# Performance work log

Hardware: AMD Instinct MI355X
Metric: run time of the kernel (lower is better)

Reference implementation:

```python
import jax, jax.numpy as jnp
import numpy as np

EMBED_DIM = 1024
NUM_HEADS = 16
HEAD_DIM = EMBED_DIM // NUM_HEADS
MAX_SEQ_LEN = 2048
B, T = 2, 2048


def setup_inputs() -> dict:
    key = jax.random.key(0)
    ks = jax.random.split(key, 12)
    d = EMBED_DIM
    s = lambda fan_in: 1.0 / np.sqrt(fan_in)
    return {
        "x": jax.random.normal(ks[0], (B, T, d), dtype=jnp.float32),
        "ln1_g": jnp.ones((d,), jnp.float32),
        "ln1_b": jnp.zeros((d,), jnp.float32),
        "w_attn": jax.random.normal(ks[1], (d, 3 * d), jnp.float32) * s(d),
        "b_attn": jnp.zeros((3 * d,), jnp.float32),
        "w_proj": jax.random.normal(ks[2], (d, d), jnp.float32) * s(d),
        "b_proj": jnp.zeros((d,), jnp.float32),
        "ln2_g": jnp.ones((d,), jnp.float32),
        "ln2_b": jnp.zeros((d,), jnp.float32),
        "w_fc": jax.random.normal(ks[3], (d, 4 * d), jnp.float32) * s(d),
        "b_fc": jnp.zeros((4 * d,), jnp.float32),
        "w_fc2": jax.random.normal(ks[4], (4 * d, d), jnp.float32) * s(4 * d),
        "b_fc2": jnp.zeros((d,), jnp.float32),
    }


def _layernorm(x, g, b, eps=1e-5):
    mu = jnp.mean(x, axis=-1, keepdims=True)
    var = jnp.var(x, axis=-1, keepdims=True)
    return (x - mu) * jax.lax.rsqrt(var + eps) * g + b


def _attention(x, w_attn, b_attn, w_proj, b_proj):
    b, t, c = x.shape
    qkv = x @ w_attn + b_attn  # [B,T,3C]
    q, k, v = jnp.split(qkv, 3, axis=-1)
    # [B,T,C] -> [B,H,T,Dh]
    rs = lambda a: a.reshape(b, t, NUM_HEADS, HEAD_DIM).transpose(0, 2, 1, 3)
    q, k, v = rs(q), rs(k), rs(v)
    wei = jnp.einsum("bhqd,bhkd->bhqk", q, k) * (HEAD_DIM ** -0.5)
    causal = jnp.tril(jnp.ones((t, t), bool))
    wei = jnp.where(causal, wei, -jnp.inf)
    wei = jax.nn.softmax(wei, axis=-1)  # attn_dropout is identity in eval mode
    out = jnp.einsum("bhqk,bhkd->bhqd", wei, v)
    out = out.transpose(0, 2, 1, 3).reshape(b, t, c)
    return out @ w_proj + b_proj  # resid_dropout identity in eval mode


def _ffn(x, w_fc, b_fc, w_fc2, b_fc2):
    h = jax.nn.gelu(x @ w_fc + b_fc, approximate=False)
    return h @ w_fc2 + b_fc2  # dropout identity in eval mode


def reference(x, ln1_g, ln1_b, w_attn, b_attn, w_proj, b_proj,
              ln2_g, ln2_b, w_fc, b_fc, w_fc2, b_fc2):
    x = x + _attention(_layernorm(x, ln1_g, ln1_b), w_attn, b_attn, w_proj, b_proj)
    x = x + _ffn(_layernorm(x, ln2_g, ln2_b), w_fc, b_fc, w_fc2, b_fc2)
    return x
```

## Files before the change

kernel.cpp:

```cpp
#include <hip/hip_runtime.h>

#define EMBED 1024
#define THREE_EMBED 3072
#define HEADS 16
#define HDIM 64
#define SEQ 2048
#define BATCH 2
#define MTOT 4096

typedef short bf16x8 __attribute__((ext_vector_type(8)));
typedef float f32x4 __attribute__((ext_vector_type(4)));

#define MFMA16(a, b, c) __builtin_amdgcn_mfma_f32_16x16x32_bf16(a, b, c, 0, 0, 0)

__device__ __forceinline__ unsigned short f2bf(float f) {
  union { float f; unsigned int u; } v; v.f = f;
  unsigned int r = v.u + 0x7fffu + ((v.u >> 16) & 1u);
  return (unsigned short)(r >> 16);
}

__device__ __forceinline__ void gload_lds16(const unsigned short* g, unsigned short* l) {
  __builtin_amdgcn_global_load_lds(
      (const __attribute__((address_space(1))) void*)g,
      (__attribute__((address_space(3))) void*)l, 16, 0, 0);
}

__device__ __forceinline__ void wait_vm0_barrier() {
  asm volatile("s_waitcnt vmcnt(0)" ::: "memory");
  __builtin_amdgcn_s_barrier();
}

__global__ __launch_bounds__(256) void k_transpose_bf16(
    const float* __restrict__ in, unsigned short* __restrict__ out, int K, int N) {
  __shared__ float t[32][33];
  int tx = threadIdx.x & 31, ty = threadIdx.x >> 5;
  int n0 = blockIdx.x * 32, k0 = blockIdx.y * 32;
#pragma unroll
  for (int i = 0; i < 32; i += 8)
    t[ty + i][tx] = in[(size_t)(k0 + ty + i) * N + n0 + tx];
  __syncthreads();
#pragma unroll
  for (int i = 0; i < 32; i += 8)
    out[(size_t)(n0 + ty + i) * K + k0 + tx] = f2bf(t[tx][ty + i]);
}

__global__ __launch_bounds__(256) void k_transpose_v(
    const unsigned short* __restrict__ qkv, unsigned short* __restrict__ Vt) {
  __shared__ unsigned short t[32][33];
  int tx = threadIdx.x & 31, ty = threadIdx.x >> 5;
  int t0 = blockIdx.x * 32;
  int d0 = (blockIdx.y & 1) * 32;
  int bh = blockIdx.y >> 1;
  int b = bh >> 4, h = bh & 15;
  const unsigned short* src = qkv + (size_t)b * SEQ * THREE_EMBED + 2 * EMBED + h * HDIM;
#pragma unroll
  for (int i = 0; i < 32; i += 8)
    t[ty + i][tx] = src[(size_t)(t0 + ty + i) * THREE_EMBED + d0 + tx];
  __syncthreads();
  unsigned short* dst = Vt + (size_t)bh * HDIM * SEQ;
#pragma unroll
  for (int i = 0; i < 32; i += 8)
    dst[(size_t)(d0 + ty + i) * SEQ + t0 + tx] = t[tx][ty + i];
}

__global__ __launch_bounds__(256) void k_layernorm(
    const float* __restrict__ x, const float* __restrict__ g,
    const float* __restrict__ b, unsigned short* __restrict__ out) {
  int row = blockIdx.x;
  int tid = threadIdx.x;
  const float4 xv = *(const float4*)(x + (size_t)row * EMBED + tid * 4);
  float s = xv.x + xv.y + xv.z + xv.w;
  float sq = xv.x * xv.x + xv.y * xv.y + xv.z * xv.z + xv.w * xv.w;
#pragma unroll
  for (int off = 1; off < 64; off <<= 1) {
    s += __shfl_xor(s, off);
    sq += __shfl_xor(sq, off);
  }
  __shared__ float red[8];
  int w = tid >> 6;
  if ((tid & 63) == 0) { red[w] = s; red[4 + w] = sq; }
  __syncthreads();
  s = red[0] + red[1] + red[2] + red[3];
  sq = red[4] + red[5] + red[6] + red[7];
  float mu = s * (1.0f / EMBED);
  float var = sq * (1.0f / EMBED) - mu * mu;
  float rs = rsqrtf(var + 1e-5f);
  float xs[4] = {xv.x, xv.y, xv.z, xv.w};
  unsigned short o[4];
#pragma unroll
  for (int c = 0; c < 4; c++) {
    int col = tid * 4 + c;
    o[c] = f2bf((xs[c] - mu) * rs * g[col] + b[col]);
  }
  *(ushort4*)(out + (size_t)row * EMBED + tid * 4) = *(const ushort4*)o;
}

template <int EPI, int BN>
__global__ __launch_bounds__(256) void k_gemm(
    const unsigned short* __restrict__ A, const unsigned short* __restrict__ Bt,
    const float* __restrict__ bias, const float* __restrict__ resid,
    float* __restrict__ outf, unsigned short* __restrict__ outb,
    int M, int N, int K) {
  constexpr int BCH = BN / 16;
  constexpr int CHUNKS = 8 + BCH;
  constexpr int CPW = CHUNKS / 4;
  constexpr int MI = (BN == 128) ? 4 : 2;
  constexpr int NJ = 4;
  __shared__ unsigned short lA[2][128 * 32];
  __shared__ unsigned short lB[2][BN * 32];
  int tid = threadIdx.x;
  int nwg = gridDim.x * gridDim.y;
  int bid = blockIdx.y * gridDim.x + blockIdx.x;
  int swz = (bid & 7) * (nwg >> 3) + (bid >> 3);
  int m0 = (swz / gridDim.x) * 128, n0 = (swz % gridDim.x) * BN;
  int lane = tid & 63, w = tid >> 6;
  int wm = (BN == 128) ? (w >> 1) * 64 : w * 32;
  int wn = (BN == 128) ? (w & 1) * 64 : 0;
  int lr = lane & 15, lg = lane >> 4;
  f32x4 acc[MI][NJ] = {};
  int scol = ((lane & 3) ^ ((lane >> 3) & 3)) * 8;
  const unsigned short* gsrc[CPW];
  int loff[CPW];
  bool isa[CPW];
#pragma unroll
  for (int c0 = 0; c0 < CPW; c0++) {
    int c = w * CPW + c0;
    if (c < 8) {
      int row = c * 16 + (lane >> 2);
      gsrc[c0] = A + (size_t)(m0 + row) * K + scol;
      loff[c0] = c * 512;
      isa[c0] = true;
    } else {
      int row = (c - 8) * 16 + (lane >> 2);
      gsrc[c0] = Bt + (size_t)(n0 + row) * K + scol;
      loff[c0] = (c - 8) * 512;
      isa[c0] = false;
    }
  }
  auto stage = [&](int k0, int cur) {
#pragma unroll
    for (int c0 = 0; c0 < CPW; c0++)
      gload_lds16(gsrc[c0] + k0, isa[c0] ? &lA[cur][loff[c0]] : &lB[cur][loff[c0]]);
  };
  int fcol = (lg ^ ((lr >> 1) & 3)) * 8;
  int nt = K >> 5;
  stage(0, 0);
  wait_vm0_barrier();
  int cur = 0;
  for (int t = 0; t < nt; t++) {
    if (t + 1 < nt) stage((t + 1) * 32, cur ^ 1);
    bf16x8 af[MI], bfr[NJ];
#pragma unroll
    for (int i = 0; i < MI; i++)
      af[i] = *(const bf16x8*)&lA[cur][(wm + i * 16 + lr) * 32 + fcol];
#pragma unroll
    for (int j = 0; j < NJ; j++)
      bfr[j] = *(const bf16x8*)&lB[cur][(wn + j * 16 + lr) * 32 + fcol];
#pragma unroll
    for (int i = 0; i < MI; i++)
#pragma unroll
      for (int j = 0; j < NJ; j++)
        acc[i][j] = MFMA16(af[i], bfr[j], acc[i][j]);
    wait_vm0_barrier();
    cur ^= 1;
  }
#pragma unroll
  for (int i = 0; i < MI; i++) {
#pragma unroll
    for (int j = 0; j < NJ; j++) {
      int colb = n0 + wn + j * 16 + lr;
      float bv = bias[colb];
#pragma unroll
      for (int r = 0; r < 4; r++) {
        int row = m0 + wm + i * 16 + lg * 4 + r;
        float v = acc[i][j][r] + bv;
        size_t idx = (size_t)row * N + colb;
        if constexpr (EPI == 0) {
          outb[idx] = f2bf(v);
        } else if constexpr (EPI == 1) {
          outf[idx] = v + resid[idx];
        } else {
          float gv = 0.5f * v * (1.0f + erff(v * 0.70710678118654752f));
          outb[idx] = f2bf(gv);
        }
      }
    }
  }
}

__global__ __launch_bounds__(256) void k_attention(
    const unsigned short* __restrict__ qkv, const unsigned short* __restrict__ Vt,
    unsigned short* __restrict__ out) {
  __shared__ unsigned short lK[2][64 * 64];
  __shared__ unsigned short lV[2][64 * 64];
  __shared__ unsigned short lP[4][16][72];
  int bid = blockIdx.x;
  int i = bid >> 3;
  int qt = 31 - (i >> 2);
  int bh = (bid & 7) * 4 + (i & 3);
  int b = bh >> 4, h = bh & 15;
  int tid = threadIdx.x, lane = tid & 63, w = tid >> 6;
  int lr = lane & 15, lg = lane >> 4;
  const unsigned short* base = qkv + (size_t)b * SEQ * THREE_EMBED + h * HDIM;
  const unsigned short* Kb = base + EMBED;
  const unsigned short* Vb = Vt + (size_t)bh * HDIM * SEQ;
  int q0 = qt * 64 + w * 16;
  bf16x8 qf[2];
  {
    int qrow = q0 + lr;
    qf[0] = *(const bf16x8*)(base + (size_t)qrow * THREE_EMBED + lg * 8);
    qf[1] = *(const bf16x8*)(base + (size_t)qrow * THREE_EMBED + 32 + lg * 8);
  }
  bf16x8 ones;
  {
    short o1 = 0x3F80;
#pragma unroll
    for (int j = 0; j < 8; j++) ones[j] = o1;
  }
  f32x4 o[4] = {};
  f32x4 osum = {};
  float m_[4] = {-INFINITY, -INFINITY, -INFINITY, -INFINITY};
  int srow = lane >> 3;
  int scol = ((lane & 7) ^ (lane >> 3)) * 8;
  const float SCL = 0.125f * 1.4426950408889634f;
  int nkv = qt + 1;
  auto stage = [&](int kt, int cur) {
#pragma unroll
    for (int c = 0; c < 2; c++) {
      int chunk = w * 2 + c;
      int row = chunk * 8 + srow;
      gload_lds16(Kb + (size_t)(kt * 64 + row) * THREE_EMBED + scol, &lK[cur][chunk * 512]);
      gload_lds16(Vb + (size_t)row * SEQ + kt * 64 + scol, &lV[cur][chunk * 512]);
    }
  };
  stage(0, 0);
  wait_vm0_barrier();
  int cur = 0;
  for (int kt = 0; kt < nkv; kt++) {
    if (kt + 1 < nkv) stage(kt + 1, cur ^ 1);
    __builtin_amdgcn_s_setprio(1);
    f32x4 s[4];
#pragma unroll
    for (int ct = 0; ct < 4; ct++) {
      int krow = ct * 16 + lr;
      int sw = (krow & 7) << 3;
      bf16x8 k0 = *(const bf16x8*)&lK[cur][krow * 64 + ((lg * 8) ^ sw)];
      bf16x8 k1 = *(const bf16x8*)&lK[cur][krow * 64 + ((32 + lg * 8) ^ sw)];
      f32x4 z = {};
      z = MFMA16(qf[0], k0, z);
      s[ct] = MFMA16(qf[1], k1, z);
    }
    __builtin_amdgcn_s_setprio(0);
    bool maskt = (kt * 64 + 63 > q0);
    float pm[4] = {-INFINITY, -INFINITY, -INFINITY, -INFINITY};
#pragma unroll
    for (int ct = 0; ct < 4; ct++) {
#pragma unroll
      for (int r = 0; r < 4; r++) {
        float sv = s[ct][r] * SCL;
        if (maskt) {
          int kg = kt * 64 + ct * 16 + lr;
          int qg = q0 + lg * 4 + r;
          if (kg > qg) sv = -INFINITY;
        }
        s[ct][r] = sv;
        pm[r] = fmaxf(pm[r], sv);
      }
    }
    float dm = fmaxf(fmaxf(pm[0] - m_[0], pm[1] - m_[1]),
                     fmaxf(pm[2] - m_[2], pm[3] - m_[3]));
    if (!__all(dm <= 8.0f)) {
#pragma unroll
      for (int r = 0; r < 4; r++) {
        float mx = pm[r];
        mx = fmaxf(mx, __shfl_xor(mx, 1));
        mx = fmaxf(mx, __shfl_xor(mx, 2));
        mx = fmaxf(mx, __shfl_xor(mx, 4));
        mx = fmaxf(mx, __shfl_xor(mx, 8));
        float mn = fmaxf(m_[r], mx);
        float al = exp2f(m_[r] - mn);
        m_[r] = mn;
        osum[r] *= al;
#pragma unroll
        for (int dt = 0; dt < 4; dt++) o[dt][r] *= al;
      }
    }
#pragma unroll
    for (int ct = 0; ct < 4; ct++)
#pragma unroll
      for (int r = 0; r < 4; r++)
        lP[w][lg * 4 + r][ct * 16 + lr] = f2bf(exp2f(s[ct][r] - m_[r]));
    __builtin_amdgcn_s_setprio(1);
#pragma unroll
    for (int ks = 0; ks < 2; ks++) {
      bf16x8 pf = *(const bf16x8*)&lP[w][lr][ks * 32 + lg * 8];
      osum = MFMA16(pf, ones, osum);
#pragma unroll
      for (int dt = 0; dt < 4; dt++) {
        int vrow = dt * 16 + lr;
        int sw = (vrow & 7) << 3;
        bf16x8 vf = *(const bf16x8*)&lV[cur][vrow * 64 + ((ks * 32 + lg * 8) ^ sw)];
        o[dt] = MFMA16(pf, vf, o[dt]);
      }
    }
    __builtin_amdgcn_s_setprio(0);
    wait_vm0_barrier();
    cur ^= 1;
  }
#pragma unroll
  for (int dt = 0; dt < 4; dt++)
#pragma unroll
    for (int r = 0; r < 4; r++) {
      int row = q0 + lg * 4 + r;
      float val = o[dt][r] / osum[r];
      out[(size_t)(b * SEQ + row) * EMBED + h * HDIM + dt * 16 + lr] = f2bf(val);
    }
}

extern "C" void kernel_launch(void* const* d_in, const int* in_sizes, int n_in,
                              void* d_out, int out_size, void* d_ws, size_t ws_size,
                              hipStream_t stream) {
  const float* x      = (const float*)d_in[0];
  const float* ln1_g  = (const float*)d_in[1];
  const float* ln1_b  = (const float*)d_in[2];
  const float* w_attn = (const float*)d_in[3];
  const float* b_attn = (const float*)d_in[4];
  const float* w_proj = (const float*)d_in[5];
  const float* b_proj = (const float*)d_in[6];
  const float* ln2_g  = (const float*)d_in[7];
  const float* ln2_b  = (const float*)d_in[8];
  const float* w_fc   = (const float*)d_in[9];
  const float* b_fc   = (const float*)d_in[10];
  const float* w_fc2  = (const float*)d_in[11];
  const float* b_fc2  = (const float*)d_in[12];
  float* outp = (float*)d_out;

  char* ws = (char*)d_ws;
  unsigned short* wT_attn = (unsigned short*)(ws);
  unsigned short* wT_proj = (unsigned short*)(ws + 6291456);
  unsigned short* wT_fc   = (unsigned short*)(ws + 8388608);
  unsigned short* wT_fc2  = (unsigned short*)(ws + 16777216);
  unsigned short* buf1    = (unsigned short*)(ws + 25165824);
  float*          x1      = (float*)(ws + 33554432);
  unsigned short* Vt      = (unsigned short*)(ws + 33554432);
  unsigned short* qkv_h   = (unsigned short*)(ws + 50331648);

  dim3 blk(256);
  k_transpose_bf16<<<dim3(3072 / 32, 1024 / 32), blk, 0, stream>>>(w_attn, wT_attn, 1024, 3072);
  k_transpose_bf16<<<dim3(1024 / 32, 1024 / 32), blk, 0, stream>>>(w_proj, wT_proj, 1024, 1024);
  k_transpose_bf16<<<dim3(4096 / 32, 1024 / 32), blk, 0, stream>>>(w_fc, wT_fc, 1024, 4096);
  k_transpose_bf16<<<dim3(1024 / 32, 4096 / 32), blk, 0, stream>>>(w_fc2, wT_fc2, 4096, 1024);
  k_layernorm<<<dim3(MTOT), blk, 0, stream>>>(x, ln1_g, ln1_b, buf1);
  k_gemm<0, 128><<<dim3(THREE_EMBED / 128, MTOT / 128), blk, 0, stream>>>(
      buf1, wT_attn, b_attn, nullptr, nullptr, qkv_h, MTOT, THREE_EMBED, EMBED);
  k_transpose_v<<<dim3(SEQ / 32, 2 * BATCH * HEADS), blk, 0, stream>>>(qkv_h, Vt);
  k_attention<<<dim3(1024), blk, 0, stream>>>(qkv_h, Vt, buf1);
  k_gemm<1, 64><<<dim3(EMBED / 64, MTOT / 128), blk, 0, stream>>>(
      buf1, wT_proj, b_proj, x, x1, nullptr, MTOT, EMBED, EMBED);
  k_layernorm<<<dim3(MTOT), blk, 0, stream>>>(x1, ln2_g, ln2_b, buf1);
  k_gemm<2, 128><<<dim3(4 * EMBED / 128, MTOT / 128), blk, 0, stream>>>(
      buf1, wT_fc, b_fc, nullptr, nullptr, qkv_h, MTOT, 4 * EMBED, EMBED);
  k_gemm<1, 64><<<dim3(EMBED / 64, MTOT / 128), blk, 0, stream>>>(
      qkv_h, wT_fc2, b_fc2, x1, outp, nullptr, MTOT, EMBED, 4 * EMBED);
}
```

Before: 279.3 us.

## Add 256x256-tile 8-wave GEMM with staged prefetch for QKV and FC1

Adds a new GEMM kernel using 256x256 output tiles, 512 threads (8 waves), a K-step of 64 and a swizzled LDS layout. Global-to-LDS loads for the next K tile are split into four stages interleaved with quarter-tile MFMA phases, separated by barriers and s_setprio. It replaces the 128-tile kernel for the QKV projection and the FC1+GELU GEMM, aiming for more operand reuse and better overlap of loads with MFMA. In exchange the grid is smaller (192 and 256 workgroups), which may underfill the GPU's CUs, and the many barriers may stall waves.

```diff
diff --git a/kernel.cpp b/kernel.cpp
--- a/kernel.cpp
+++ b/kernel.cpp
@@ -93,6 +93,140 @@
     o[c] = f2bf((xs[c] - mu) * rs * g[col] + b[col]);
   }
   *(ushort4*)(out + (size_t)row * EMBED + tid * 4) = *(const ushort4*)o;
+}
+
+template <int EPI>
+__global__ __launch_bounds__(512, 2) void k_gemm8(
+    const unsigned short* __restrict__ A, const unsigned short* __restrict__ Bt,
+    const float* __restrict__ bias, const float* __restrict__ resid,
+    float* __restrict__ outf, unsigned short* __restrict__ outb,
+    int M, int N, int K) {
+  __shared__ unsigned short lA[2][16384];
+  __shared__ unsigned short lB[2][16384];
+  int tid = threadIdx.x;
+  int nwg = gridDim.x * gridDim.y;
+  int bid = blockIdx.y * gridDim.x + blockIdx.x;
+  int swz = (bid & 7) * (nwg >> 3) + (bid >> 3);
+  int m0 = (swz / gridDim.x) * 256, n0 = (swz % gridDim.x) * 256;
+  int lane = tid & 63, w = tid >> 6;
+  int lr = lane & 15, lg = lane >> 4;
+  int warow = (w >> 2) * 64;
+  int wbrow = (w & 3) * 32;
+  int rx = lr & 7;
+  int colk[2] = {(lg ^ rx) * 8, ((4 + lg) ^ rx) * 8};
+  f32x4 acc[8][4] = {};
+  int swzk = ((lane & 7) ^ ((lane >> 3) & 7)) * 8;
+  const unsigned short* gA[2];
+  const unsigned short* gB[2];
+#pragma unroll
+  for (int i = 0; i < 2; i++) {
+    int chrow = (w * 2 + i) * 8 + (lane >> 3);
+    gA[i] = A + (size_t)(m0 + chrow) * K + swzk;
+    gB[i] = Bt + (size_t)(n0 + chrow) * K + swzk;
+  }
+  int NT = K >> 6;
+  auto stage1 = [&](int sel, int kt, int nxt) {
+    int h = sel >> 1;
+    size_t goff = (size_t)(h * 128) * K + (size_t)kt * 64;
+    int lo = h * 8192 + w * 1024;
+    if ((sel & 1) == 0) {
+      gload_lds16(gA[0] + goff, &lA[nxt][lo]);
+      gload_lds16(gA[1] + goff, &lA[nxt][lo + 512]);
+    } else {
+      gload_lds16(gB[0] + goff, &lB[nxt][lo]);
+      gload_lds16(gB[1] + goff, &lB[nxt][lo + 512]);
+    }
+  };
+  bf16x8 afr[4][2], bfr[2][2];
+  auto dsrd = [&](int cur, int mh, int nh) {
+#pragma unroll
+    for (int ii = 0; ii < 4; ii++) {
+      int ra = mh * 128 + warow + ii * 16 + lr;
+#pragma unroll
+      for (int ks = 0; ks < 2; ks++)
+        afr[ii][ks] = *(const bf16x8*)&lA[cur][ra * 64 + colk[ks]];
+    }
+#pragma unroll
+    for (int jj = 0; jj < 2; jj++) {
+      int rb = nh * 128 + wbrow + jj * 16 + lr;
+#pragma unroll
+      for (int ks = 0; ks < 2; ks++)
+        bfr[jj][ks] = *(const bf16x8*)&lB[cur][rb * 64 + colk[ks]];
+    }
+  };
+  auto domfma = [&](int mh, int nh) {
+    __builtin_amdgcn_s_setprio(1);
+#pragma unroll
+    for (int ii = 0; ii < 4; ii++)
+#pragma unroll
+      for (int jj = 0; jj < 2; jj++)
+#pragma unroll
+        for (int ks = 0; ks < 2; ks++)
+          acc[mh * 4 + ii][nh * 2 + jj] =
+              MFMA16(afr[ii][ks], bfr[jj][ks], acc[mh * 4 + ii][nh * 2 + jj]);
+    __builtin_amdgcn_s_setprio(0);
+  };
+  stage1(0, 0, 0); stage1(1, 0, 0); stage1(2, 0, 0); stage1(3, 0, 0);
+  wait_vm0_barrier();
+  for (int t = 0; t < NT - 1; t++) {
+    int cur = t & 1, nxt = cur ^ 1;
+    dsrd(cur, 0, 0); stage1(0, t + 1, nxt);
+    asm volatile("s_waitcnt vmcnt(4)" ::: "memory");
+    __builtin_amdgcn_s_barrier();
+    domfma(0, 0);
+    __builtin_amdgcn_s_barrier();
+    dsrd(cur, 1, 0); stage1(1, t + 1, nxt);
+    asm volatile("s_waitcnt vmcnt(4)" ::: "memory");
+    __builtin_amdgcn_s_barrier();
+    domfma(1, 0);
+    __builtin_amdgcn_s_barrier();
+    dsrd(cur, 0, 1); stage1(2, t + 1, nxt);
+    __builtin_amdgcn_s_barrier();
+    domfma(0, 1);
+    __builtin_amdgcn_s_barrier();
+    dsrd(cur, 1, 1); stage1(3, t + 1, nxt);
+    asm volatile("s_waitcnt vmcnt(4)" ::: "memory");
+    __builtin_amdgcn_s_barrier();
+    domfma(1, 1);
+    __builtin_amdgcn_s_barrier();
+  }
+  {
+    int cur = (NT - 1) & 1;
+    dsrd(cur, 0, 0);
+    asm volatile("s_waitcnt vmcnt(2)" ::: "memory");
+    __builtin_amdgcn_s_barrier();
+    domfma(0, 0);
+    __builtin_amdgcn_s_barrier();
+    dsrd(cur, 1, 0);
+    asm volatile("s_waitcnt vmcnt(0)" ::: "memory");
+    __builtin_amdgcn_s_barrier();
+    domfma(1, 0);
+    __builtin_amdgcn_s_barrier();
+    dsrd(cur, 0, 1); domfma(0, 1);
+    dsrd(cur, 1, 1); domfma(1, 1);
+  }
+#pragma unroll
+  for (int i = 0; i < 8; i++) {
+#pragma unroll
+    for (int j = 0; j < 4; j++) {
+      int col = n0 + (j >> 1) * 128 + wbrow + (j & 1) * 16 + lr;
+      float bv = bias[col];
+#pragma unroll
+      for (int r = 0; r < 4; r++) {
+        int row = m0 + (i >> 2) * 128 + warow + (i & 3) * 16 + lg * 4 + r;
+        float v = acc[i][j][r] + bv;
+        size_t idx = (size_t)row * N + col;
+        if constexpr (EPI == 0) {
+          outb[idx] = f2bf(v);
+        } else if constexpr (EPI == 1) {
+          outf[idx] = v + resid[idx];
+        } else {
+          float gv = 0.5f * v * (1.0f + erff(v * 0.70710678118654752f));
+          outb[idx] = f2bf(gv);
+        }
+      }
+    }
+  }
 }
 
 template <int EPI, int BN>
@@ -351,14 +485,14 @@
   k_transpose_bf16<<<dim3(4096 / 32, 1024 / 32), blk, 0, stream>>>(w_fc, wT_fc, 1024, 4096);
   k_transpose_bf16<<<dim3(1024 / 32, 4096 / 32), blk, 0, stream>>>(w_fc2, wT_fc2, 4096, 1024);
   k_layernorm<<<dim3(MTOT), blk, 0, stream>>>(x, ln1_g, ln1_b, buf1);
-  k_gemm<0, 128><<<dim3(THREE_EMBED / 128, MTOT / 128), blk, 0, stream>>>(
+  k_gemm8<0><<<dim3(THREE_EMBED / 256, MTOT / 256), dim3(512), 0, stream>>>(
       buf1, wT_attn, b_attn, nullptr, nullptr, qkv_h, MTOT, THREE_EMBED, EMBED);
   k_transpose_v<<<dim3(SEQ / 32, 2 * BATCH * HEADS), blk, 0, stream>>>(qkv_h, Vt);
   k_attention<<<dim3(1024), blk, 0, stream>>>(qkv_h, Vt, buf1);
   k_gemm<1, 64><<<dim3(EMBED / 64, MTOT / 128), blk, 0, stream>>>(
       buf1, wT_proj, b_proj, x, x1, nullptr, MTOT, EMBED, EMBED);
   k_layernorm<<<dim3(MTOT), blk, 0, stream>>>(x1, ln2_g, ln2_b, buf1);
-  k_gemm<2, 128><<<dim3(4 * EMBED / 128, MTOT / 128), blk, 0, stream>>>(
+  k_gemm8<2><<<dim3(4 * EMBED / 256, MTOT / 256), dim3(512), 0, stream>>>(
       buf1, wT_fc, b_fc, nullptr, nullptr, qkv_h, MTOT, 4 * EMBED, EMBED);
   k_gemm<1, 64><<<dim3(EMBED / 64, MTOT / 128), blk, 0, stream>>>(
       qkv_h, wT_fc2, b_fc2, x1, outp, nullptr, MTOT, EMBED, 4 * EMBED);
```

Result: no change. 283.9 us (+1.7%).

## Triple-buffer GEMM LDS staging with partial vmcnt waits and MFMA priority

Applied to the files above, without the earlier changes.

The bf16 GEMM's K loop moves from double to triple buffering in LDS. Loads are issued two tiles ahead and the loop waits only until the older tile's loads finish (vmcnt(CPW)) instead of draining all outstanding loads each iteration. MFMA blocks are also wrapped in s_setprio to favour the math wave. This aims to hide global-to-LDS latency better, at the cost of more LDS per block, which may lower occupancy.

```diff
diff --git a/kernel.cpp b/kernel.cpp
--- a/kernel.cpp
+++ b/kernel.cpp
@@ -28,6 +28,17 @@
 __device__ __forceinline__ void wait_vm0_barrier() {
   asm volatile("s_waitcnt vmcnt(0)" ::: "memory");
   __builtin_amdgcn_s_barrier();
+}
+
+template <int N>
+__device__ __forceinline__ void wait_vmcnt() {
+  if constexpr (N == 0) asm volatile("s_waitcnt vmcnt(0)" ::: "memory");
+  else if constexpr (N == 1) asm volatile("s_waitcnt vmcnt(1)" ::: "memory");
+  else if constexpr (N == 2) asm volatile("s_waitcnt vmcnt(2)" ::: "memory");
+  else if constexpr (N == 3) asm volatile("s_waitcnt vmcnt(3)" ::: "memory");
+  else if constexpr (N == 4) asm volatile("s_waitcnt vmcnt(4)" ::: "memory");
+  else if constexpr (N == 6) asm volatile("s_waitcnt vmcnt(6)" ::: "memory");
+  else if constexpr (N == 8) asm volatile("s_waitcnt vmcnt(8)" ::: "memory");
 }
 
 __global__ __launch_bounds__(256) void k_transpose_bf16(
@@ -106,8 +117,8 @@
   constexpr int CPW = CHUNKS / 4;
   constexpr int MI = (BN == 128) ? 4 : 2;
   constexpr int NJ = 4;
-  __shared__ unsigned short lA[2][128 * 32];
-  __shared__ unsigned short lB[2][BN * 32];
+  __shared__ unsigned short lA[3][128 * 32];
+  __shared__ unsigned short lB[3][BN * 32];
   int tid = threadIdx.x;
   int nwg = gridDim.x * gridDim.y;
   int bid = blockIdx.y * gridDim.x + blockIdx.x;
@@ -137,33 +148,45 @@
       isa[c0] = false;
     }
   }
-  auto stage = [&](int k0, int cur) {
+  auto stage = [&](int k0, int buf) {
 #pragma unroll
     for (int c0 = 0; c0 < CPW; c0++)
-      gload_lds16(gsrc[c0] + k0, isa[c0] ? &lA[cur][loff[c0]] : &lB[cur][loff[c0]]);
+      gload_lds16(gsrc[c0] + k0, isa[c0] ? &lA[buf][loff[c0]] : &lB[buf][loff[c0]]);
   };
   int fcol = (lg ^ ((lr >> 1) & 3)) * 8;
+  auto compute = [&](int buf) {
+    bf16x8 af[MI], bfr[NJ];
+#pragma unroll
+    for (int i = 0; i < MI; i++)
+      af[i] = *(const bf16x8*)&lA[buf][(wm + i * 16 + lr) * 32 + fcol];
+#pragma unroll
+    for (int j = 0; j < NJ; j++)
+      bfr[j] = *(const bf16x8*)&lB[buf][(wn + j * 16 + lr) * 32 + fcol];
+    __builtin_amdgcn_s_setprio(1);
+#pragma unroll
+    for (int i = 0; i < MI; i++)
+#pragma unroll
+      for (int j = 0; j < NJ; j++)
+        acc[i][j] = MFMA16(af[i], bfr[j], acc[i][j]);
+    __builtin_amdgcn_s_setprio(0);
+  };
   int nt = K >> 5;
   stage(0, 0);
-  wait_vm0_barrier();
-  int cur = 0;
-  for (int t = 0; t < nt; t++) {
-    if (t + 1 < nt) stage((t + 1) * 32, cur ^ 1);
-    bf16x8 af[MI], bfr[NJ];
-#pragma unroll
-    for (int i = 0; i < MI; i++)
-      af[i] = *(const bf16x8*)&lA[cur][(wm + i * 16 + lr) * 32 + fcol];
-#pragma unroll
-    for (int j = 0; j < NJ; j++)
-      bfr[j] = *(const bf16x8*)&lB[cur][(wn + j * 16 + lr) * 32 + fcol];
-#pragma unroll
-    for (int i = 0; i < MI; i++)
-#pragma unroll
-      for (int j = 0; j < NJ; j++)
-        acc[i][j] = MFMA16(af[i], bfr[j], acc[i][j]);
-    wait_vm0_barrier();
-    cur ^= 1;
-  }
+  stage(32, 1);
+  wait_vmcnt<CPW>();
+  __builtin_amdgcn_s_barrier();
+  int c0 = 0, c1 = 1, c2 = 2;
+  for (int t = 0; t < nt - 2; t++) {
+    stage((t + 2) * 32, c2);
+    compute(c0);
+    wait_vmcnt<CPW>();
+    __builtin_amdgcn_s_barrier();
+    int tmp = c0; c0 = c1; c1 = c2; c2 = tmp;
+  }
+  compute(c0);
+  wait_vmcnt<0>();
+  __builtin_amdgcn_s_barrier();
+  compute(c1);
 #pragma unroll
   for (int i = 0; i < MI; i++) {
 #pragma unroll
```

Measured after the change: 280.0 us. Within noise of the previous version (+0.2%).
